# Kernel optimization log

Hardware: AMD Instinct MI355X
Metric: run time of the kernel (lower is better)

The kernel has to match this reference:

```python
import jax, jax.numpy as jnp
import numpy as np

H = 128      # hidden_dim
HEADS = 4
HD = H // HEADS
B, S, D, A, I = 64, 512, 64, 3, 13


def layernorm(x, g, b, eps=1e-5):
    m = x.mean(-1, keepdims=True)
    v = ((x - m) ** 2).mean(-1, keepdims=True)
    return g * (x - m) / jnp.sqrt(v + eps) + b


def setup_inputs() -> dict:
    key = jax.random.key(0)
    ks = jax.random.split(key, 12)
    rn = lambda k, shp, s=0.05: jax.random.normal(k, shp, jnp.float32) * s
    return {
        "x": jax.random.normal(ks[0], (B, S, D), jnp.float32),
        "info": jax.random.normal(ks[1], (B, I), jnp.float32),
        "W_cell": rn(ks[2], (4 * H, D + H)), "b_cell": jnp.zeros(4 * H, jnp.float32),
        "Wqkv": rn(ks[3], (3 * H, H)), "bqkv": jnp.zeros(3 * H, jnp.float32),
        "Wo": rn(ks[4], (H, H)), "bo": jnp.zeros(H, jnp.float32),
        "ln_g": jnp.ones(H, jnp.float32), "ln_b": jnp.zeros(H, jnp.float32),
        "Wa1": rn(ks[5], (128, H + I)), "ba1": jnp.zeros(128, jnp.float32),
        "lna_g": jnp.ones(128, jnp.float32), "lna_b": jnp.zeros(128, jnp.float32),
        "Wa2": rn(ks[6], (A, 128)), "ba2": jnp.zeros(A, jnp.float32),
        "Wc1": rn(ks[7], (128, H + I)), "bc1": jnp.zeros(128, jnp.float32),
        "lnc_g": jnp.ones(128, jnp.float32), "lnc_b": jnp.zeros(128, jnp.float32),
        "Wc2": rn(ks[8], (1, 128)), "bc2": jnp.zeros(1, jnp.float32),
    }


def reference(x, info, W_cell, b_cell, Wqkv, bqkv, Wo, bo, ln_g, ln_b,
              Wa1, ba1, lna_g, lna_b, Wa2, ba2, Wc1, bc1, lnc_g, lnc_b, Wc2, bc2):
    Bx, Sx, _ = x.shape
    h0 = jnp.zeros((Bx, H), x.dtype)
    c0 = jnp.zeros((Bx, H), x.dtype)
    n0 = jnp.ones((Bx, H), x.dtype)

    def step(carry, xt):
        h, c, n = carry
        gates = jnp.concatenate([xt, h], -1) @ W_cell.T + b_cell
        i, f, o, z = jnp.split(gates, 4, axis=-1)
        i = jnp.exp(jnp.clip(i, -5.0, 5.0))
        f = jnp.exp(jnp.clip(f, -5.0, 5.0))
        c = jnp.clip(f * c + i * jnp.tanh(z), -1e6, 1e6)
        n = jnp.clip(f * n + i, 1e-6, 1e6)
        h = jnp.nan_to_num(jax.nn.sigmoid(o) * (c / n), nan=0.0, posinf=0.0, neginf=0.0)
        return (h, c, n), h

    _, hs = jax.lax.scan(step, (h0, c0, n0), jnp.swapaxes(x, 0, 1))  # (S,B,H)
    seq_h = jnp.swapaxes(hs, 0, 1)  # (B,S,H)

    # MultiheadAttention (self-attn, batch_first, shared in_proj)
    qkv = seq_h @ Wqkv.T + bqkv
    q, k, v = jnp.split(qkv, 3, -1)
    split_heads = lambda t: t.reshape(Bx, Sx, HEADS, HD).transpose(0, 2, 1, 3)
    q, k, v = split_heads(q), split_heads(k), split_heads(v)
    scores = jnp.einsum('bhqd,bhkd->bhqk', q, k) / np.sqrt(HD).astype(np.float32)
    attn = jax.nn.softmax(scores, axis=-1)
    av = jnp.einsum('bhqk,bhkd->bhqd', attn, v).transpose(0, 2, 1, 3).reshape(Bx, Sx, H)
    attn_out = av @ Wo.T + bo
    context = layernorm(seq_h + attn_out, ln_g, ln_b).mean(axis=1)  # (B,H)

    comb = jnp.concatenate([context, info], -1)  # (B, H+I)
    action_probs = jax.nn.softmax(
        jax.nn.relu(layernorm(comb @ Wa1.T + ba1, lna_g, lna_b)) @ Wa2.T + ba2, axis=-1)
    value = jax.nn.relu(layernorm(comb @ Wc1.T + bc1, lnc_g, lnc_b)) @ Wc2.T + bc2
    return (action_probs, value)
```

## Files before the change

kernel.cpp:

```cpp
#include <hip/hip_runtime.h>

typedef unsigned short ushort_t;
typedef unsigned int uint_t;

__device__ __forceinline__ float bflo(uint_t u){ union{uint_t i;float f;}v; v.i=u<<16; return v.f; }
__device__ __forceinline__ float bfhi(uint_t u){ union{uint_t i;float f;}v; v.i=u&0xffff0000u; return v.f; }
__device__ __forceinline__ float bfu(ushort_t u){ union{uint_t i;float f;}v; v.i=((uint_t)u)<<16; return v.f; }
__device__ __forceinline__ ushort_t f2b(float f){
  union{float f;uint_t i;}v; v.f=f;
  uint_t r = v.i + 0x7fffu + ((v.i>>16)&1u);
  return (ushort_t)(r>>16);
}
__device__ __forceinline__ void ld8bf(const ushort_t* p, float* w){
  uint4 u = *(const uint4*)p;
  w[0]=bflo(u.x); w[1]=bfhi(u.x); w[2]=bflo(u.y); w[3]=bfhi(u.y);
  w[4]=bflo(u.z); w[5]=bfhi(u.z); w[6]=bflo(u.w); w[7]=bfhi(u.w);
}
__device__ __forceinline__ void cvt8(uint4 u, float* d){
  d[0]=bflo(u.x); d[1]=bfhi(u.x); d[2]=bflo(u.y); d[3]=bfhi(u.y);
  d[4]=bflo(u.z); d[5]=bfhi(u.z); d[6]=bflo(u.w); d[7]=bfhi(u.w);
}
__device__ __forceinline__ float ldin(const void* p, size_t i, int isbf){
  return isbf ? bfu(((const ushort_t*)p)[i]) : ((const float*)p)[i];
}
__device__ __forceinline__ float rlane(float v, int l){
  return __uint_as_float(__builtin_amdgcn_readlane(__float_as_uint(v), l));
}

#define DOT128(acc, Wv, Bv) { float s0_=0.f,s1_=0.f,s2_=0.f,s3_=0.f; \
  _Pragma("unroll") \
  for (int k_=0;k_<128;k_+=4){ float4 h4_ = *(const float4*)&(Bv)[k_]; \
    s0_ += (Wv)[k_]*h4_.x; s1_ += (Wv)[k_+1]*h4_.y; \
    s2_ += (Wv)[k_+2]*h4_.z; s3_ += (Wv)[k_+3]*h4_.w; } \
  acc += (s0_+s1_)+(s2_+s3_); }
#define DOT64A(acc, Wv, Bv) { float s0_=0.f,s1_=0.f,s2_=0.f,s3_=0.f; \
  _Pragma("unroll") \
  for (int k_=0;k_<64;k_+=4){ float4 h4_ = *(const float4*)&(Bv)[k_]; \
    s0_ += (Wv)[k_]*h4_.x; s1_ += (Wv)[k_+1]*h4_.y; \
    s2_ += (Wv)[k_+2]*h4_.z; s3_ += (Wv)[k_+3]*h4_.w; } \
  acc += (s0_+s1_)+(s2_+s3_); }

typedef __attribute__((ext_vector_type(8))) short bf16x8;
typedef __attribute__((ext_vector_type(8))) _Float16 f16x8;
typedef __attribute__((ext_vector_type(4))) float f32x4;
__device__ __forceinline__ bf16x8 bcast8(uint4 u){ return __builtin_bit_cast(bf16x8, u); }
__device__ __forceinline__ f16x8  hcast8(uint4 u){ return __builtin_bit_cast(f16x8, u); }
__device__ __forceinline__ bf16x8 cvt8bf(const float* p){
  float4 a = *(const float4*)p; float4 b = *(const float4*)(p+4);
  uint4 u;
  u.x = (uint_t)f2b(a.x) | ((uint_t)f2b(a.y)<<16);
  u.y = (uint_t)f2b(a.z) | ((uint_t)f2b(a.w)<<16);
  u.z = (uint_t)f2b(b.x) | ((uint_t)f2b(b.y)<<16);
  u.w = (uint_t)f2b(b.z) | ((uint_t)f2b(b.w)<<16);
  return bcast8(u);
}
__device__ __forceinline__ void cvt8hl(const float* p, bf16x8* hi, bf16x8* lo){
  float v[8];
  *(float4*)&v[0] = *(const float4*)p;
  *(float4*)&v[4] = *(const float4*)(p+4);
  ushort_t h[8], l[8];
  #pragma unroll
  for (int j=0;j<8;++j){ h[j] = f2b(v[j]); l[j] = f2b(v[j] - bfu(h[j])); }
  uint4 uh = { (uint_t)h[0]|((uint_t)h[1]<<16), (uint_t)h[2]|((uint_t)h[3]<<16),
               (uint_t)h[4]|((uint_t)h[5]<<16), (uint_t)h[6]|((uint_t)h[7]<<16) };
  uint4 ul = { (uint_t)l[0]|((uint_t)l[1]<<16), (uint_t)l[2]|((uint_t)l[3]<<16),
               (uint_t)l[4]|((uint_t)l[5]<<16), (uint_t)l[6]|((uint_t)l[7]<<16) };
  *hi = bcast8(uh); *lo = bcast8(ul);
}
__device__ __forceinline__ ushort_t f2h(float f){
  _Float16 h = (_Float16)f;
  return __builtin_bit_cast(ushort_t, h);
}
__device__ __forceinline__ float h2f(ushort_t u){
  _Float16 h = __builtin_bit_cast(_Float16, u);
  return (float)h;
}

__global__ void k_detect(const uint_t* __restrict__ lng_raw, int* __restrict__ flag){
  if (threadIdx.x == 0) *flag = (lng_raw[0] == 0x3F803F80u) ? 1 : 0;
}

__global__ __launch_bounds__(256) void k_cvtw(const float* __restrict__ Wq,
    const float* __restrict__ Wo, const float* __restrict__ Wc,
    ushort_t* __restrict__ wqb, ushort_t* __restrict__ wob,
    ushort_t* __restrict__ wxh, ushort_t* __restrict__ wxl,
    ushort_t* __restrict__ whf, ushort_t* __restrict__ whl,
    const int* __restrict__ flag){
  if (*flag == 1) return;
  int i = blockIdx.x*256 + threadIdx.x;
  if (i < 12288){
    float4 f = ((const float4*)Wq)[i];
    uint2 u = { (uint_t)f2b(f.x) | ((uint_t)f2b(f.y)<<16),
                (uint_t)f2b(f.z) | ((uint_t)f2b(f.w)<<16) };
    ((uint2*)wqb)[i] = u;
  } else if (i < 16384){
    int k = i - 12288;
    float4 f = ((const float4*)Wo)[k];
    uint2 u = { (uint_t)f2b(f.x) | ((uint_t)f2b(f.y)<<16),
                (uint_t)f2b(f.z) | ((uint_t)f2b(f.w)<<16) };
    ((uint2*)wob)[k] = u;
  } else if (i < 24576){
    int k = i - 16384;
    int j = k >> 4, kq = (k & 15)*4;
    float4 f = *(const float4*)(Wc + (size_t)j*192 + kq);
    ushort_t h0=f2b(f.x), h1=f2b(f.y), h2=f2b(f.z), h3=f2b(f.w);
    ushort_t l0=f2b(f.x-bfu(h0)), l1=f2b(f.y-bfu(h1));
    ushort_t l2=f2b(f.z-bfu(h2)), l3=f2b(f.w-bfu(h3));
    ((uint2*)(wxh + (size_t)j*64 + kq))[0] = { (uint_t)h0|((uint_t)h1<<16), (uint_t)h2|((uint_t)h3<<16) };
    ((uint2*)(wxl + (size_t)j*64 + kq))[0] = { (uint_t)l0|((uint_t)l1<<16), (uint_t)l2|((uint_t)l3<<16) };
  } else if (i < 32768){
    int k2 = i - 24576;
    int j = k2 >> 4, kc = (k2 & 15)*8;
    const float* src = Wc + (size_t)j*192 + 64 + kc;
    ushort_t hh[8], ll[8];
    #pragma unroll
    for (int q=0;q<8;++q){
      hh[q] = f2h(src[q]);
      ll[q] = f2h(src[q] - h2f(hh[q]));
    }
    uint4 uh = { (uint_t)hh[0]|((uint_t)hh[1]<<16), (uint_t)hh[2]|((uint_t)hh[3]<<16),
                 (uint_t)hh[4]|((uint_t)hh[5]<<16), (uint_t)hh[6]|((uint_t)hh[7]<<16) };
    uint4 ul = { (uint_t)ll[0]|((uint_t)ll[1]<<16), (uint_t)ll[2]|((uint_t)ll[3]<<16),
                 (uint_t)ll[4]|((uint_t)ll[5]<<16), (uint_t)ll[6]|((uint_t)ll[7]<<16) };
    *(uint4*)(whf + (size_t)j*136 + kc) = uh;
    *(uint4*)(whl + (size_t)j*128 + kc) = ul;
  }
}

__global__ __launch_bounds__(256) void k_gx_bf(const void* __restrict__ x,
    const void* __restrict__ Wc, const void* __restrict__ bc,
    float* __restrict__ gx, const int* __restrict__ flag){
  if (*flag == 0) return;
  __shared__ float xs[2048];
  int row0 = blockIdx.x*32, t = threadIdx.x;
  {
    uint4 u = ((const uint4*)((const ushort_t*)x + (size_t)row0*64))[t];
    cvt8(u, &xs[t*8]);
  }
  __syncthreads();
  for (int pass=0; pass<2; ++pass){
    int j = t + pass*256;
    float w[64];
    const ushort_t* wr = (const ushort_t*)Wc + (size_t)j*192;
    #pragma unroll
    for (int q=0;q<8;q++) ld8bf(wr + 8*q, &w[8*q]);
    float bj = bfu(((const ushort_t*)bc)[j]);
    for (int s=0;s<32;++s){
      float acc = bj;
      DOT64A(acc, w, &xs[s*64]);
      gx[(size_t)(row0+s)*512 + j] = acc;
    }
  }
}

__global__ __launch_bounds__(256) void k_gx_f32(const float* __restrict__ x,
    const float* __restrict__ bc,
    const ushort_t* __restrict__ wxh, const ushort_t* __restrict__ wxl,
    float* __restrict__ gx, const int* __restrict__ flag){
  if (*flag == 1) return;
  int t = threadIdx.x, lane = t & 63, wave = t >> 6;
  int l16 = lane & 15, quad = lane >> 4;
  int rowb = blockIdx.x*64 + wave*16;
  const float* xp = x + (size_t)(rowb + l16)*64;
  bf16x8 xh0, xl0, xh1, xl1;
  cvt8hl(xp + quad*8,      &xh0, &xl0);
  cvt8hl(xp + 32 + quad*8, &xh1, &xl1);
  int r0 = rowb + quad*4;
  for (int ct=0; ct<32; ++ct){
    int j = ct*16 + l16;
    const ushort_t* bh = wxh + (size_t)j*64 + quad*8;
    const ushort_t* bl = wxl + (size_t)j*64 + quad*8;
    bf16x8 wh0 = bcast8(*(const uint4*)(bh));
    bf16x8 wh1 = bcast8(*(const uint4*)(bh + 32));
    bf16x8 wl0 = bcast8(*(const uint4*)(bl));
    bf16x8 wl1 = bcast8(*(const uint4*)(bl + 32));
    f32x4 acc = {0.f,0.f,0.f,0.f};
    acc = __builtin_amdgcn_mfma_f32_16x16x32_bf16(xh0, wh0, acc, 0,0,0);
    acc = __builtin_amdgcn_mfma_f32_16x16x32_bf16(xh1, wh1, acc, 0,0,0);
    acc = __builtin_amdgcn_mfma_f32_16x16x32_bf16(xh0, wl0, acc, 0,0,0);
    acc = __builtin_amdgcn_mfma_f32_16x16x32_bf16(xh1, wl1, acc, 0,0,0);
    acc = __builtin_amdgcn_mfma_f32_16x16x32_bf16(xl0, wh0, acc, 0,0,0);
    acc = __builtin_amdgcn_mfma_f32_16x16x32_bf16(xl1, wh1, acc, 0,0,0);
    float bj = bc[j];
    #pragma unroll
    for (int r=0;r<4;++r)
      gx[(size_t)(r0+r)*512 + j] = acc[r] + bj;
  }
}

__global__ __attribute__((amdgpu_flat_work_group_size(512,512), amdgpu_waves_per_eu(2,2)))
void k_rec_hl(const ushort_t* __restrict__ whf,
    const ushort_t* __restrict__ whl,
    const float* __restrict__ gx, float* __restrict__ seq_h,
    const int* __restrict__ flag){
  if (*flag == 1) return;
  int b = blockIdx.x, t = threadIdx.x;
  int lane = t & 63, wv = t >> 6, l16 = lane & 15, quad = lane >> 4;
  __shared__ ushort_t wlds[512*136];
  __shared__ float gs[512];
  __shared__ ushort_t hz[384];
  {
    const uint4* src = (const uint4*)whf;
    uint4* dst = (uint4*)wlds;
    for (int i=t; i<8704; i+=512) dst[i] = src[i];
  }
  if (t < 384) hz[t] = (ushort_t)0;
  const float* gxb = gx + (size_t)b*512*512;
  float g0=0.f,g1=0.f,g2=0.f,g3=0.f;
  float c = 0.f, n = 1.f;
  if (t < 128){
    g0 = gxb[t]; g1 = gxb[128+t]; g2 = gxb[256+t]; g3 = gxb[384+t];
  }
  float* shout = seq_h + (size_t)b*512*128;
  __syncthreads();
  const int c0 = 4*wv, c1 = 4*wv+1, c2 = 4*wv+2, c3 = 4*wv+3;
  const ushort_t* w0 = wlds + (c0*16 + l16)*136 + quad*8;
  const ushort_t* w1 = wlds + (c1*16 + l16)*136 + quad*8;
  const ushort_t* w2 = wlds + (c2*16 + l16)*136 + quad*8;
  const ushort_t* w3 = wlds + (c3*16 + l16)*136 + quad*8;
  const ushort_t* p0 = whl + (size_t)(c0*16 + l16)*128 + quad*8;
  const ushort_t* p1 = whl + (size_t)(c1*16 + l16)*128 + quad*8;
  const ushort_t* p2 = whl + (size_t)(c2*16 + l16)*128 + quad*8;
  const ushort_t* p3 = whl + (size_t)(c3*16 + l16)*128 + quad*8;
#define BDECL(T, ptr) uint4 T##0 = *(const uint4*)(ptr), T##1 = *(const uint4*)((ptr)+32), \
  T##2 = *(const uint4*)((ptr)+64), T##3 = *(const uint4*)((ptr)+96);
  BDECL(U0, w0) BDECL(U1, w1) BDECL(U2, w2) BDECL(U3, w3)
  BDECL(V0, p0) BDECL(V1, p1) BDECL(V2, p2) BDECL(V3, p3)
#undef BDECL
#define UPIN(U) asm volatile("" : "+v"(U.x), "+v"(U.y), "+v"(U.z), "+v"(U.w));
  UPIN(U00) UPIN(U01) UPIN(U02) UPIN(U03)
  UPIN(U10) UPIN(U11) UPIN(U12) UPIN(U13)
  UPIN(U20) UPIN(U21) UPIN(U22) UPIN(U23)
  UPIN(U30) UPIN(U31) UPIN(U32) UPIN(U33)
  UPIN(V00) UPIN(V01) UPIN(V02) UPIN(V03)
  UPIN(V10) UPIN(V11) UPIN(V12) UPIN(V13)
  UPIN(V20) UPIN(V21) UPIN(V22) UPIN(V23)
  UPIN(V30) UPIN(V31) UPIN(V32) UPIN(V33)
#undef UPIN
  const ushort_t* hzsel = hz + ((l16 < 2) ? l16*128 : 256) + quad*8;
  for (int ts=0; ts<512; ++ts){
    f16x8 A0 = hcast8(*(const uint4*)(hzsel));
    f16x8 A1 = hcast8(*(const uint4*)(hzsel + 32));
    f16x8 A2 = hcast8(*(const uint4*)(hzsel + 64));
    f16x8 A3 = hcast8(*(const uint4*)(hzsel + 96));
    f32x4 s0 = {0.f,0.f,0.f,0.f}, s1 = {0.f,0.f,0.f,0.f};
    f32x4 s2 = {0.f,0.f,0.f,0.f}, s3 = {0.f,0.f,0.f,0.f};
#define TILE(sa, Uf, Vf) \
    sa = __builtin_amdgcn_mfma_f32_16x16x32_f16(A0, hcast8(Uf##0), sa, 0,0,0); \
    sa = __builtin_amdgcn_mfma_f32_16x16x32_f16(A1, hcast8(Uf##1), sa, 0,0,0); \
    sa = __builtin_amdgcn_mfma_f32_16x16x32_f16(A2, hcast8(Uf##2), sa, 0,0,0); \
    sa = __builtin_amdgcn_mfma_f32_16x16x32_f16(A3, hcast8(Uf##3), sa, 0,0,0); \
    sa = __builtin_amdgcn_mfma_f32_16x16x32_f16(A0, hcast8(Vf##0), sa, 0,0,0); \
    sa = __builtin_amdgcn_mfma_f32_16x16x32_f16(A1, hcast8(Vf##1), sa, 0,0,0); \
    sa = __builtin_amdgcn_mfma_f32_16x16x32_f16(A2, hcast8(Vf##2), sa, 0,0,0); \
    sa = __builtin_amdgcn_mfma_f32_16x16x32_f16(A3, hcast8(Vf##3), sa, 0,0,0);
    TILE(s0, U0, V0)
    TILE(s1, U1, V1)
    TILE(s2, U2, V2)
    TILE(s3, U3, V3)
#undef TILE
    if (quad == 0){
      gs[c0*16 + l16] = s0[0] + s0[1];
      gs[c1*16 + l16] = s1[0] + s1[1];
      gs[c2*16 + l16] = s2[0] + s2[1];
      gs[c3*16 + l16] = s3[0] + s3[1];
    }
    __syncthreads();
    if (t < 128){
      float gi = gs[t]     + g0;
      float gf = gs[128+t] + g1;
      float go = gs[256+t] + g2;
      float gz = gs[384+t] + g3;
      if (ts+1 < 512){
        const float* gn = gxb + (size_t)(ts+1)*512;
        g0 = gn[t]; g1 = gn[128+t]; g2 = gn[256+t]; g3 = gn[384+t];
      }
      float ii = __expf(fminf(fmaxf(gi,-5.f),5.f));
      float ff = __expf(fminf(fmaxf(gf,-5.f),5.f));
      float e2 = __expf(2.f*gz);
      float zt = 1.f - 2.f/(e2+1.f);
      c = fminf(fmaxf(ff*c + ii*zt, -1e6f), 1e6f);
      n = fminf(fmaxf(ff*n + ii, 1e-6f), 1e6f);
      float oo = 1.f/(1.f+__expf(-go));
      float h = oo*(c/n);
      if (!isfinite(h)) h = 0.f;
      shout[(size_t)ts*128 + t] = h;
      ushort_t hhi = f2h(h);
      hz[t] = hhi;
      hz[128+t] = f2h(h - h2f(hhi));
    }
    __syncthreads();
  }
}

__global__ __launch_bounds__(1024, 4) void k_rec_bf(const void* __restrict__ Wc,
    const float* __restrict__ gx, float* __restrict__ seq_h,
    const int* __restrict__ flag){
  if (*flag == 0) return;
  int b = blockIdx.x, t = threadIdx.x;
  int lane = t & 63, j = t & 511, half = t >> 9;
  __shared__ float ps[1024];
  __shared__ float hs[128];
  uint_t wu[32];
  {
    const uint4* wp = (const uint4*)((const ushort_t*)Wc + (size_t)j*192 + 64 + 64*half);
    #pragma unroll
    for (int q=0;q<8;q++){ uint4 u = wp[q];
      wu[4*q]=u.x; wu[4*q+1]=u.y; wu[4*q+2]=u.z; wu[4*q+3]=u.w; }
  }
  const float* gxb = gx + (size_t)b*512*512;
  float g0=0.f, g1=0.f;
  if (half==0){ g0 = gxb[j]; g1 = gxb[512 + j]; }
  float hreg = 0.f;
  float c = 0.f, n = 1.f;
  float* shout = seq_h + (size_t)b*512*128;
  for (int ts=0; ts<512; ++ts){
    float a0, a1=0.f, a2=0.f, a3=0.f;
    if (half==0){
      a0 = g0; g0 = g1;
      g1 = (ts+2 < 512) ? gxb[(size_t)(ts+2)*512 + j] : 0.f;
    } else a0 = 0.f;
    #pragma unroll
    for (int kk=0; kk<32; kk+=2){
      float h0v = rlane(hreg, 2*kk),   h1v = rlane(hreg, 2*kk+1);
      float h2v = rlane(hreg, 2*kk+2), h3v = rlane(hreg, 2*kk+3);
      a0 = fmaf(bflo(wu[kk]),   h0v, a0);
      a1 = fmaf(bfhi(wu[kk]),   h1v, a1);
      a2 = fmaf(bflo(wu[kk+1]), h2v, a2);
      a3 = fmaf(bfhi(wu[kk+1]), h3v, a3);
    }
    ps[t] = (a0+a1)+(a2+a3);
    __syncthreads();
    if (t < 128){
      float gi = ps[t]     + ps[512+t];
      float gf = ps[128+t] + ps[640+t];
      float go = ps[256+t] + ps[768+t];
      float gz = ps[384+t] + ps[896+t];
      float ii = __expf(fminf(fmaxf(gi,-5.f),5.f));
      float ff = __expf(fminf(fmaxf(gf,-5.f),5.f));
      float e2 = __expf(2.f*gz);
      float zt = 1.f - 2.f/(e2+1.f);
      c = fminf(fmaxf(ff*c + ii*zt, -1e6f), 1e6f);
      n = fminf(fmaxf(ff*n + ii, 1e-6f), 1e6f);
      float oo = 1.f/(1.f+__expf(-go));
      float h = oo*(c/n);
      if (!isfinite(h)) h = 0.f;
      hs[t] = h;
      shout[(size_t)ts*128 + t] = h;
    }
    __syncthreads();
    hreg = hs[(half<<6) | lane];
  }
}

__global__ __launch_bounds__(512) void k_rec_inl(const void* __restrict__ x,
    const void* __restrict__ Wc, const void* __restrict__ bc,
    float* __restrict__ seq_h, const int* __restrict__ flag){
  int isbf = *flag;
  int b = blockIdx.x, j = threadIdx.x;
  __shared__ float hs[128];
  __shared__ float gs[512];
  __shared__ float xr[4][64];
  float w[128], wx[64];
  if (isbf){
    const ushort_t* wr = (const ushort_t*)Wc + (size_t)j*192;
    #pragma unroll
    for (int q=0;q<8;q++)  ld8bf(wr + 8*q, &wx[8*q]);
    #pragma unroll
    for (int q=0;q<16;q++) ld8bf(wr + 64 + 8*q, &w[8*q]);
  } else {
    const float* wr = (const float*)Wc + (size_t)j*192;
    #pragma unroll
    for (int q=0;q<16;q++){ float4 f=*(const float4*)(wr+4*q);
      wx[4*q]=f.x; wx[4*q+1]=f.y; wx[4*q+2]=f.z; wx[4*q+3]=f.w; }
    #pragma unroll
    for (int q=0;q<32;q++){ float4 f=*(const float4*)(wr+64+4*q);
      w[4*q]=f.x; w[4*q+1]=f.y; w[4*q+2]=f.z; w[4*q+3]=f.w; }
  }
  float bj = ldin(bc, j, isbf);
  float c = 0.f, n = 1.f;
  if (j < 128) hs[j] = 0.f;
  if (j < 128){
    int r = j>>6, k = j&63;
    xr[r][k] = ldin(x, ((size_t)b*512 + r)*64 + k, isbf);
  }
  __syncthreads();
  for (int t=0; t<512; ++t){
    const float* xt = xr[t&3];
    float acc = bj;
    DOT64A(acc, wx, xt);
    DOT128(acc, w, hs);
    gs[j] = acc;
    __syncthreads();
    if (j < 128){
      float gi=gs[j], gf=gs[128+j], go=gs[256+j], gz=gs[384+j];
      float ii = __expf(fminf(fmaxf(gi,-5.f),5.f));
      float ff = __expf(fminf(fmaxf(gf,-5.f),5.f));
      float e2 = __expf(2.f*gz);
      float zt = 1.f - 2.f/(e2+1.f);
      c = fminf(fmaxf(ff*c + ii*zt, -1e6f), 1e6f);
      n = fminf(fmaxf(ff*n + ii, 1e-6f), 1e6f);
      float oo = 1.f/(1.f+__expf(-go));
      float h = oo*(c/n);
      if (!isfinite(h)) h = 0.f;
      hs[j] = h;
      seq_h[((size_t)b*512 + t)*128 + j] = h;
    } else if (j >= 448 && (t+2) < 512){
      int k = j & 63;
      xr[(t+2)&3][k] = ldin(x, ((size_t)b*512 + (t+2))*64 + k, isbf);
    }
    __syncthreads();
  }
}

__global__ __launch_bounds__(256) void k_qkv(const float* __restrict__ seq_h,
    const void* __restrict__ Wq, const void* __restrict__ bq,
    const ushort_t* __restrict__ wqb,
    ushort_t* __restrict__ qkv, const int* __restrict__ flag){
  int isbf = *flag;
  int row0 = blockIdx.x*32, t = threadIdx.x;
  if (isbf){
    __shared__ float hsb[4096];
    {
      const float4* hp = (const float4*)(seq_h + (size_t)row0*128);
      #pragma unroll
      for (int i=t;i<1024;i+=256) ((float4*)hsb)[i] = hp[i];
    }
    __syncthreads();
    for (int pass=0; pass<2; ++pass){
      int j = (pass==0) ? t : 256 + t;
      if (j >= 384) break;
      float w[128];
      const ushort_t* wr = (const ushort_t*)Wq + (size_t)j*128;
      #pragma unroll
      for (int q=0;q<16;q++) ld8bf(wr + 8*q, &w[8*q]);
      float bj = bfu(((const ushort_t*)bq)[j]);
      for (int s=0;s<32;++s){
        float acc = bj;
        DOT128(acc, w, &hsb[s*128]);
        qkv[(size_t)(row0+s)*384 + j] = f2b(acc);
      }
    }
  } else {
    int lane = t & 63, wave = t >> 6, l16 = lane & 15, quad = lane >> 4;
    int rt = wave & 1, chalf = wave >> 1;
    int rowg = row0 + rt*16 + l16;
    const float* hp = seq_h + (size_t)rowg*128 + quad*8;
    bf16x8 A0 = cvt8bf(hp);
    bf16x8 A1 = cvt8bf(hp + 32);
    bf16x8 A2 = cvt8bf(hp + 64);
    bf16x8 A3 = cvt8bf(hp + 96);
    int rbase = row0 + rt*16 + quad*4;
    for (int ci=0; ci<12; ++ci){
      int ct = chalf*12 + ci;
      int col = ct*16 + l16;
      const ushort_t* wb = wqb + (size_t)col*128 + quad*8;
      f32x4 acc = {0.f,0.f,0.f,0.f};
      acc = __builtin_amdgcn_mfma_f32_16x16x32_bf16(A0, bcast8(*(const uint4*)(wb)),      acc, 0,0,0);
      acc = __builtin_amdgcn_mfma_f32_16x16x32_bf16(A1, bcast8(*(const uint4*)(wb + 32)), acc, 0,0,0);
      acc = __builtin_amdgcn_mfma_f32_16x16x32_bf16(A2, bcast8(*(const uint4*)(wb + 64)), acc, 0,0,0);
      acc = __builtin_amdgcn_mfma_f32_16x16x32_bf16(A3, bcast8(*(const uint4*)(wb + 96)), acc, 0,0,0);
      float bj = ((const float*)bq)[col];
      #pragma unroll
      for (int r=0;r<4;++r)
        qkv[(size_t)(rbase+r)*384 + col] = f2b(acc[r] + bj);
    }
  }
}

#define AROW4(OP) OP(0) OP(1) OP(2) OP(3)
__global__ __launch_bounds__(512) void k_attn(const ushort_t* __restrict__ qkv,
    ushort_t* __restrict__ av){
  int b = blockIdx.x >> 2, h = blockIdx.x & 3;
  int t = threadIdx.x, lane = t & 63, wave = t >> 6;
  int l16 = lane & 15, quad = lane >> 4;
  __shared__ ushort_t Vt[32*512];
  __shared__ ushort_t Pl[8*16*64];
  const ushort_t* base = qkv + (size_t)b*512*384 + h*32;
  {
    const ushort_t* vr = base + (size_t)t*384 + 256;
    ushort_t tmp[32];
    *(uint4*)&tmp[0]  = *(const uint4*)(vr);
    *(uint4*)&tmp[8]  = *(const uint4*)(vr+8);
    *(uint4*)&tmp[16] = *(const uint4*)(vr+16);
    *(uint4*)&tmp[24] = *(const uint4*)(vr+24);
    #pragma unroll
    for (int d=0; d<32; ++d) Vt[d*512 + t] = tmp[d];
  }
  __syncthreads();
  ushort_t* Pw = Pl + wave*16*64;
  const float scale = 0.17677669529663687f;
  for (int q4=0; q4<4; ++q4){
    int qt = wave + q4*8;
    bf16x8 qa;
    { uint4 u = *(const uint4*)(base + (size_t)(qt*16 + l16)*384 + quad*8);
      qa = bcast8(u); }
    f32x4 O0 = {0.f,0.f,0.f,0.f}, O1 = {0.f,0.f,0.f,0.f};
    float m0=-1e30f,m1=-1e30f,m2=-1e30f,m3=-1e30f;
    float l0=0.f,l1=0.f,l2=0.f,l3=0.f;
    for (int ch=0; ch<8; ++ch){
      f32x4 S0,S1,S2,S3;
      {
        const ushort_t* kb = base + 128 + quad*8;
        uint4 u0 = *(const uint4*)(kb + (size_t)(ch*64 +  0 + l16)*384);
        uint4 u1 = *(const uint4*)(kb + (size_t)(ch*64 + 16 + l16)*384);
        uint4 u2 = *(const uint4*)(kb + (size_t)(ch*64 + 32 + l16)*384);
        uint4 u3 = *(const uint4*)(kb + (size_t)(ch*64 + 48 + l16)*384);
        f32x4 z = {0.f,0.f,0.f,0.f};
        S0 = __builtin_amdgcn_mfma_f32_16x16x32_bf16(qa, bcast8(u0), z, 0,0,0);
        S1 = __builtin_amdgcn_mfma_f32_16x16x32_bf16(qa, bcast8(u1), z, 0,0,0);
        S2 = __builtin_amdgcn_mfma_f32_16x16x32_bf16(qa, bcast8(u2), z, 0,0,0);
        S3 = __builtin_amdgcn_mfma_f32_16x16x32_bf16(qa, bcast8(u3), z, 0,0,0);
      }
#define CMAX(r) float c##r = fmaxf(fmaxf(S0[r],S1[r]), fmaxf(S2[r],S3[r])) * scale; \
      c##r = fmaxf(c##r, __shfl_xor(c##r,1)); c##r = fmaxf(c##r, __shfl_xor(c##r,2)); \
      c##r = fmaxf(c##r, __shfl_xor(c##r,4)); c##r = fmaxf(c##r, __shfl_xor(c##r,8)); \
      float M##r = fmaxf(m##r, c##r); float al##r = __expf(m##r - M##r); \
      m##r = M##r; O0[r] *= al##r; O1[r] *= al##r; l##r *= al##r;
      AROW4(CMAX)
#undef CMAX
#define PEXP(r) float ps##r; { \
      float p0 = __expf(S0[r]*scale - m##r); \
      float p1 = __expf(S1[r]*scale - m##r); \
      float p2 = __expf(S2[r]*scale - m##r); \
      float p3 = __expf(S3[r]*scale - m##r); \
      ps##r = (p0+p1)+(p2+p3); \
      Pw[(quad*4+(r))*64 +  0 + l16] = f2b(p0); \
      Pw[(quad*4+(r))*64 + 16 + l16] = f2b(p1); \
      Pw[(quad*4+(r))*64 + 32 + l16] = f2b(p2); \
      Pw[(quad*4+(r))*64 + 48 + l16] = f2b(p3); }
      AROW4(PEXP)
#undef PEXP
#define PSUM(r) ps##r += __shfl_xor(ps##r,1); ps##r += __shfl_xor(ps##r,2); \
      ps##r += __shfl_xor(ps##r,4); ps##r += __shfl_xor(ps##r,8); l##r += ps##r;
      AROW4(PSUM)
#undef PSUM
      asm volatile("s_waitcnt lgkmcnt(0)" ::: "memory");
      bf16x8 pa0, pa1;
      { uint4 u = *(const uint4*)&Pw[l16*64 + quad*8];      pa0 = bcast8(u); }
      { uint4 u = *(const uint4*)&Pw[l16*64 + 32 + quad*8]; pa1 = bcast8(u); }
      {
        uint4 v0 = *(const uint4*)&Vt[(l16)*512    + ch*64 + quad*8];
        uint4 v1 = *(const uint4*)&Vt[(l16)*512    + ch*64 + 32 + quad*8];
        uint4 v2 = *(const uint4*)&Vt[(16+l16)*512 + ch*64 + quad*8];
        uint4 v3 = *(const uint4*)&Vt[(16+l16)*512 + ch*64 + 32 + quad*8];
        O0 = __builtin_amdgcn_mfma_f32_16x16x32_bf16(pa0, bcast8(v0), O0, 0,0,0);
        O0 = __builtin_amdgcn_mfma_f32_16x16x32_bf16(pa1, bcast8(v1), O0, 0,0,0);
        O1 = __builtin_amdgcn_mfma_f32_16x16x32_bf16(pa0, bcast8(v2), O1, 0,0,0);
        O1 = __builtin_amdgcn_mfma_f32_16x16x32_bf16(pa1, bcast8(v3), O1, 0,0,0);
      }
    }
#define OST(r) { float iv = 1.f/l##r; int row = qt*16 + quad*4 + (r); \
      ushort_t* op = av + (size_t)(b*512 + row)*128 + h*32; \
      op[l16]      = f2b(O0[r]*iv); \
      op[16 + l16] = f2b(O1[r]*iv); }
    AROW4(OST)
#undef OST
  }
}

__global__ __launch_bounds__(256) void k_ctx(const ushort_t* __restrict__ av,
    const float* __restrict__ seq_h, const void* __restrict__ Wo,
    const void* __restrict__ bo_, const void* __restrict__ lng,
    const void* __restrict__ lnb, const ushort_t* __restrict__ wob,
    float* __restrict__ partial, const int* __restrict__ flag){
  int isbf = *flag;
  __shared__ float rs[4096];
  __shared__ float mrow[32], srow[32];
  __shared__ float halfsum[128];
  int row0 = blockIdx.x*32, t = threadIdx.x;
  int j = t & 127, sh = t >> 7;
  if (isbf){
    __shared__ float avs[4096];
    {
      const uint4* ap = (const uint4*)(av + (size_t)row0*128);
      for (int i=t;i<512;i+=256) cvt8(ap[i], &avs[i*8]);
    }
    __syncthreads();
    float w[128];
    const ushort_t* wr = (const ushort_t*)Wo + (size_t)j*128;
    #pragma unroll
    for (int q=0;q<16;q++) ld8bf(wr + 8*q, &w[8*q]);
    float bj = bfu(((const ushort_t*)bo_)[j]);
    for (int si=0; si<16; ++si){
      int s = sh*16 + si;
      float acc = bj;
      DOT128(acc, w, &avs[s*128]);
      rs[s*128+j] = acc + seq_h[(size_t)(row0+s)*128 + j];
    }
  } else {
    int lane = t & 63, wave = t >> 6, l16 = lane & 15, quad = lane >> 4;
    int rt = wave & 1, chalf = wave >> 1;
    int rowg = row0 + rt*16 + l16;
    const ushort_t* ap = av + (size_t)rowg*128 + quad*8;
    bf16x8 A0 = bcast8(*(const uint4*)(ap));
    bf16x8 A1 = bcast8(*(const uint4*)(ap + 32));
    bf16x8 A2 = bcast8(*(const uint4*)(ap + 64));
    bf16x8 A3 = bcast8(*(const uint4*)(ap + 96));
    int rl0 = rt*16 + quad*4;
    for (int ci=0; ci<4; ++ci){
      int ct = chalf*4 + ci;
      int col = ct*16 + l16;
      const ushort_t* wb = wob + (size_t)col*128 + quad*8;
      f32x4 acc = {0.f,0.f,0.f,0.f};
      acc = __builtin_amdgcn_mfma_f32_16x16x32_bf16(A0, bcast8(*(const uint4*)(wb)),      acc, 0,0,0);
      acc = __builtin_amdgcn_mfma_f32_16x16x32_bf16(A1, bcast8(*(const uint4*)(wb + 32)), acc, 0,0,0);
      acc = __builtin_amdgcn_mfma_f32_16x16x32_bf16(A2, bcast8(*(const uint4*)(wb + 64)), acc, 0,0,0);
      acc = __builtin_amdgcn_mfma_f32_16x16x32_bf16(A3, bcast8(*(const uint4*)(wb + 96)), acc, 0,0,0);
      float bj2 = ((const float*)bo_)[col];
      #pragma unroll
      for (int r=0;r<4;++r){
        int rl = rl0 + r;
        rs[rl*128 + col] = acc[r] + bj2 + seq_h[(size_t)(row0+rl)*128 + col];
      }
    }
  }
  __syncthreads();
  {
    int rr = t>>3, part = t&7;
    float vals[16], sm = 0.f;
    #pragma unroll
    for (int k2=0;k2<16;k2++){ vals[k2] = rs[rr*128 + part + 8*k2]; sm += vals[k2]; }
    sm += __shfl_xor(sm,1); sm += __shfl_xor(sm,2); sm += __shfl_xor(sm,4);
    float mean = sm*(1.f/128.f);
    float vv = 0.f;
    #pragma unroll
    for (int k2=0;k2<16;k2++){ float d = vals[k2]-mean; vv += d*d; }
    vv += __shfl_xor(vv,1); vv += __shfl_xor(vv,2); vv += __shfl_xor(vv,4);
    if (part==0){ mrow[rr]=mean; srow[rr]=rsqrtf(vv*(1.f/128.f)+1e-5f); }
  }
  __syncthreads();
  float g = ldin(lng, j, isbf), bb = ldin(lnb, j, isbf);
  float accs = 0.f;
  for (int si=0; si<16; ++si){
    int s = sh*16 + si;
    accs += g*(rs[s*128+j]-mrow[s])*srow[s] + bb;
  }
  if (sh==0) halfsum[j] = accs;
  __syncthreads();
  if (sh==1){
    int bidx = row0>>9, tile = (row0>>5)&15;
    partial[((size_t)bidx*16 + tile)*128 + j] = halfsum[j] + accs;
  }
}

__global__ __launch_bounds__(128) void k_head(const float* __restrict__ partial,
    const void* __restrict__ info,
    const void* Wa1, const void* ba1, const void* lnag, const void* lnab,
    const void* Wa2, const void* ba2,
    const void* Wc1, const void* bc1, const void* lncg, const void* lncb,
    const void* Wc2, const void* bc2, void* __restrict__ out,
    const int* __restrict__ flag){
  int isbf = *flag;
  int b = blockIdx.x, t = threadIdx.x;
  __shared__ float comb[144];
  __shared__ float red[128];
  __shared__ float uu[128];
  float s = 0.f;
  #pragma unroll
  for (int i=0;i<16;i++) s += partial[((size_t)b*16+i)*128 + t];
  comb[t] = s*(1.f/512.f);
  if (t < 13) comb[128+t] = ldin(info, (size_t)b*13+t, isbf);
  __syncthreads();
  for (int br=0; br<2; ++br){
    const void* W1 = br ? Wc1 : Wa1;
    const void* b1 = br ? bc1 : ba1;
    const void* lg_ = br ? lncg : lnag;
    const void* lb_ = br ? lncb : lnab;
    float a = ldin(b1, t, isbf);
    for (int k=0;k<141;k++) a += ldin(W1, (size_t)t*141+k, isbf)*comb[k];
    red[t] = a; __syncthreads();
    for (int st=64; st>0; st>>=1){ if (t<st) red[t]+=red[t+st]; __syncthreads(); }
    float mean = red[0]*(1.f/128.f);
    __syncthreads();
    float d = a - mean;
    red[t] = d*d; __syncthreads();
    for (int st=64; st>0; st>>=1){ if (t<st) red[t]+=red[t+st]; __syncthreads(); }
    float rstd = rsqrtf(red[0]*(1.f/128.f)+1e-5f);
    __syncthreads();
    float u = ldin(lg_, t, isbf)*d*rstd + ldin(lb_, t, isbf);
    uu[t] = fmaxf(u, 0.f);
    __syncthreads();
    if (br==0){
      if (t < 3){
        float lg2 = ldin(ba2, t, isbf);
        for (int k=0;k<128;k++) lg2 += ldin(Wa2, (size_t)t*128+k, isbf)*uu[k];
        red[t] = lg2;
      }
      __syncthreads();
      if (t==0){
        float mx = fmaxf(red[0], fmaxf(red[1], red[2]));
        float e0=__expf(red[0]-mx), e1=__expf(red[1]-mx), e2=__expf(red[2]-mx);
        float inv = 1.f/(e0+e1+e2);
        if (isbf){
          ushort_t* o = (ushort_t*)out;
          o[b*3+0]=f2b(e0*inv); o[b*3+1]=f2b(e1*inv); o[b*3+2]=f2b(e2*inv);
        } else {
          float* o = (float*)out;
          o[b*3+0]=e0*inv; o[b*3+1]=e1*inv; o[b*3+2]=e2*inv;
        }
      }
      __syncthreads();
    } else {
      if (t==0){
        float v = ldin(bc2, 0, isbf);
        for (int k=0;k<128;k++) v += ldin(Wc2, k, isbf)*uu[k];
        if (isbf) ((ushort_t*)out)[192 + b] = f2b(v);
        else      ((float*)out)[192 + b] = v;
      }
    }
  }
}

extern "C" void kernel_launch(void* const* d_in, const int* in_sizes, int n_in,
                              void* d_out, int out_size, void* d_ws, size_t ws_size,
                              hipStream_t stream){
  const void* x    = d_in[0];
  const void* info = d_in[1];
  const void* Wcell= d_in[2];
  const void* bcell= d_in[3];
  const void* Wqkv = d_in[4];
  const void* bqkv = d_in[5];
  const void* Wo   = d_in[6];
  const void* bo   = d_in[7];
  const void* lng  = d_in[8];
  const void* lnb  = d_in[9];
  const void* Wa1  = d_in[10];
  const void* ba1  = d_in[11];
  const void* lnag = d_in[12];
  const void* lnab = d_in[13];
  const void* Wa2  = d_in[14];
  const void* ba2  = d_in[15];
  const void* Wc1  = d_in[16];
  const void* bc1  = d_in[17];
  const void* lncg = d_in[18];
  const void* lncb = d_in[19];
  const void* Wc2  = d_in[20];
  const void* bc2  = d_in[21];

  char* ws = (char*)d_ws;
  const int bigws = (ws_size >= ((size_t)82<<20)) ? 1 : 0;
  float*    seqh = (float*)   ws;
  float*    gxf  = (float*)   (ws + ((size_t)16<<20));
  ushort_t* qkv  = (ushort_t*)(ws + ((size_t)16<<20));
  ushort_t* av   = (ushort_t*)(ws + ((size_t)40<<20));
  float*    part = (float*)   (ws + ((size_t)48<<20));
  int*      flag = bigws ? (int*)(ws + ((size_t)80<<20))
                         : (int*)(ws + ((size_t)48<<20) + (512<<10));
  ushort_t* wqb  = (ushort_t*)(ws + ((size_t)80<<20) + (1<<20));
  ushort_t* wob  = wqb + 384*128;
  ushort_t* wxh  = wob + 128*128;
  ushort_t* wxl  = wxh + 512*64;
  ushort_t* whf  = wxl + 512*64;
  ushort_t* whl  = whf + 512*136;

  k_detect<<<1, 64, 0, stream>>>((const uint_t*)lng, flag);
  if (bigws){
    k_cvtw  <<< 128, 256, 0, stream>>>((const float*)Wqkv, (const float*)Wo,
                                       (const float*)Wcell, wqb, wob, wxh, wxl, whf, whl, flag);
    k_gx_bf <<<1024, 256, 0, stream>>>(x, Wcell, bcell, gxf, flag);
    k_gx_f32<<< 512, 256, 0, stream>>>((const float*)x, (const float*)bcell,
                                       wxh, wxl, gxf, flag);
    k_rec_bf <<< 64, 1024, 0, stream>>>(Wcell, gxf, seqh, flag);
    k_rec_hl <<< 64,  512, 0, stream>>>(whf, whl, gxf, seqh, flag);
  } else {
    k_rec_inl<<<64, 512, 0, stream>>>(x, Wcell, bcell, seqh, flag);
    k_cvtw  <<< 128, 256, 0, stream>>>((const float*)Wqkv, (const float*)Wo,
                                       (const float*)Wcell, wqb, wob, wxh, wxl, whf, whl, flag);
  }
  k_qkv <<<1024, 256, 0, stream>>>(seqh, Wqkv, bqkv, wqb, qkv, flag);
  k_attn<<< 256, 512, 0, stream>>>(qkv, av);
  k_ctx <<<1024, 256, 0, stream>>>(av, seqh, Wo, bo, lng, lnb, wob, part, flag);
  k_head<<<  64, 128, 0, stream>>>(part, info, Wa1, ba1, lnag, lnab, Wa2, ba2,
                                   Wc1, bc1, lncg, lncb, Wc2, bc2, d_out, flag);
}
```

Measured before the change: 736.1 us.

## Replicate recurrent cell update per wave to drop second barrier per step

```diff
diff --git a/kernel.cpp b/kernel.cpp
--- a/kernel.cpp
+++ b/kernel.cpp
@@ -197,31 +197,33 @@
   int b = blockIdx.x, t = threadIdx.x;
   int lane = t & 63, wv = t >> 6, l16 = lane & 15, quad = lane >> 4;
   __shared__ ushort_t wlds[512*136];
-  __shared__ float gs[512];
-  __shared__ ushort_t hz[384];
+  __shared__ float gs[2][512];
+  __shared__ ushort_t hzw[8][448];
   {
     const uint4* src = (const uint4*)whf;
     uint4* dst = (uint4*)wlds;
     for (int i=t; i<8704; i+=512) dst[i] = src[i];
   }
-  if (t < 384) hz[t] = (ushort_t)0;
+  {
+    ushort_t* mz = hzw[wv];
+    for (int i=lane; i<448; i+=64) mz[i] = (ushort_t)0;
+  }
   const float* gxb = gx + (size_t)b*512*512;
-  float g0=0.f,g1=0.f,g2=0.f,g3=0.f;
-  float c = 0.f, n = 1.f;
-  if (t < 128){
-    g0 = gxb[t]; g1 = gxb[128+t]; g2 = gxb[256+t]; g3 = gxb[384+t];
-  }
+  const int i0 = lane, i1 = 64 + lane;
+  float g00=gxb[i0], g01=gxb[128+i0], g02=gxb[256+i0], g03=gxb[384+i0];
+  float g10=gxb[i1], g11=gxb[128+i1], g12=gxb[256+i1], g13=gxb[384+i1];
+  float c0s=0.f, n0s=1.f, c1s=0.f, n1s=1.f;
   float* shout = seq_h + (size_t)b*512*128;
   __syncthreads();
-  const int c0 = 4*wv, c1 = 4*wv+1, c2 = 4*wv+2, c3 = 4*wv+3;
-  const ushort_t* w0 = wlds + (c0*16 + l16)*136 + quad*8;
-  const ushort_t* w1 = wlds + (c1*16 + l16)*136 + quad*8;
-  const ushort_t* w2 = wlds + (c2*16 + l16)*136 + quad*8;
-  const ushort_t* w3 = wlds + (c3*16 + l16)*136 + quad*8;
-  const ushort_t* p0 = whl + (size_t)(c0*16 + l16)*128 + quad*8;
-  const ushort_t* p1 = whl + (size_t)(c1*16 + l16)*128 + quad*8;
-  const ushort_t* p2 = whl + (size_t)(c2*16 + l16)*128 + quad*8;
-  const ushort_t* p3 = whl + (size_t)(c3*16 + l16)*128 + quad*8;
+  const int cc0 = 4*wv, cc1 = 4*wv+1, cc2 = 4*wv+2, cc3 = 4*wv+3;
+  const ushort_t* w0 = wlds + (cc0*16 + l16)*136 + quad*8;
+  const ushort_t* w1 = wlds + (cc1*16 + l16)*136 + quad*8;
+  const ushort_t* w2 = wlds + (cc2*16 + l16)*136 + quad*8;
+  const ushort_t* w3 = wlds + (cc3*16 + l16)*136 + quad*8;
+  const ushort_t* p0 = whl + (size_t)(cc0*16 + l16)*128 + quad*8;
+  const ushort_t* p1 = whl + (size_t)(cc1*16 + l16)*128 + quad*8;
+  const ushort_t* p2 = whl + (size_t)(cc2*16 + l16)*128 + quad*8;
+  const ushort_t* p3 = whl + (size_t)(cc3*16 + l16)*128 + quad*8;
 #define BDECL(T, ptr) uint4 T##0 = *(const uint4*)(ptr), T##1 = *(const uint4*)((ptr)+32), \
   T##2 = *(const uint4*)((ptr)+64), T##3 = *(const uint4*)((ptr)+96);
   BDECL(U0, w0) BDECL(U1, w1) BDECL(U2, w2) BDECL(U3, w3)
@@ -237,7 +239,8 @@
   UPIN(V20) UPIN(V21) UPIN(V22) UPIN(V23)
   UPIN(V30) UPIN(V31) UPIN(V32) UPIN(V33)
 #undef UPIN
-  const ushort_t* hzsel = hz + ((l16 < 2) ? l16*128 : 256) + quad*8;
+  ushort_t* myhz = hzw[wv];
+  const ushort_t* hzsel = myhz + ((l16 == 0) ? 0 : ((l16 == 1) ? 160 : 320)) + quad*8;
   for (int ts=0; ts<512; ++ts){
     f16x8 A0 = hcast8(*(const uint4*)(hzsel));
     f16x8 A1 = hcast8(*(const uint4*)(hzsel + 32));
@@ -260,36 +263,59 @@
     TILE(s3, U3, V3)
 #undef TILE
     if (quad == 0){
-      gs[c0*16 + l16] = s0[0] + s0[1];
-      gs[c1*16 + l16] = s1[0] + s1[1];
-      gs[c2*16 + l16] = s2[0] + s2[1];
-      gs[c3*16 + l16] = s3[0] + s3[1];
-    }
-    __syncthreads();
-    if (t < 128){
-      float gi = gs[t]     + g0;
-      float gf = gs[128+t] + g1;
-      float go = gs[256+t] + g2;
-      float gz = gs[384+t] + g3;
-      if (ts+1 < 512){
-        const float* gn = gxb + (size_t)(ts+1)*512;
-        g0 = gn[t]; g1 = gn[128+t]; g2 = gn[256+t]; g3 = gn[384+t];
-      }
-      float ii = __expf(fminf(fmaxf(gi,-5.f),5.f));
-      float ff = __expf(fminf(fmaxf(gf,-5.f),5.f));
-      float e2 = __expf(2.f*gz);
+      float* go = gs[ts&1];
+      go[cc0*16 + l16] = s0[0] + s0[1];
+      go[cc1*16 + l16] = s1[0] + s1[1];
+      go[cc2*16 + l16] = s2[0] + s2[1];
+      go[cc3*16 + l16] = s3[0] + s3[1];
+    }
+    __syncthreads();
+    const float* gsr = gs[ts&1];
+    float gi0 = gsr[i0]     + g00;
+    float gf0 = gsr[128+i0] + g01;
+    float go0 = gsr[256+i0] + g02;
+    float gz0 = gsr[384+i0] + g03;
+    float gi1 = gsr[i1]     + g10;
+    float gf1 = gsr[128+i1] + g11;
+    float go1 = gsr[256+i1] + g12;
+    float gz1 = gsr[384+i1] + g13;
+    if (ts+1 < 512){
+      const float* gn = gxb + (size_t)(ts+1)*512;
+      g00 = gn[i0]; g01 = gn[128+i0]; g02 = gn[256+i0]; g03 = gn[384+i0];
+      g10 = gn[i1]; g11 = gn[128+i1]; g12 = gn[256+i1]; g13 = gn[384+i1];
+    }
+    float h0, h1;
+    {
+      float ii = __expf(fminf(fmaxf(gi0,-5.f),5.f));
+      float ff = __expf(fminf(fmaxf(gf0,-5.f),5.f));
+      float e2 = __expf(2.f*gz0);
       float zt = 1.f - 2.f/(e2+1.f);
-      c = fminf(fmaxf(ff*c + ii*zt, -1e6f), 1e6f);
-      n = fminf(fmaxf(ff*n + ii, 1e-6f), 1e6f);
-      float oo = 1.f/(1.f+__expf(-go));
-      float h = oo*(c/n);
-      if (!isfinite(h)) h = 0.f;
-      shout[(size_t)ts*128 + t] = h;
-      ushort_t hhi = f2h(h);
-      hz[t] = hhi;
-      hz[128+t] = f2h(h - h2f(hhi));
-    }
-    __syncthreads();
+      c0s = fminf(fmaxf(ff*c0s + ii*zt, -1e6f), 1e6f);
+      n0s = fminf(fmaxf(ff*n0s + ii, 1e-6f), 1e6f);
+      float oo = 1.f/(1.f+__expf(-go0));
+      h0 = oo*(c0s/n0s);
+      if (!isfinite(h0)) h0 = 0.f;
+    }
+    {
+      float ii = __expf(fminf(fmaxf(gi1,-5.f),5.f));
+      float ff = __expf(fminf(fmaxf(gf1,-5.f),5.f));
+      float e2 = __expf(2.f*gz1);
+      float zt = 1.f - 2.f/(e2+1.f);
+      c1s = fminf(fmaxf(ff*c1s + ii*zt, -1e6f), 1e6f);
+      n1s = fminf(fmaxf(ff*n1s + ii, 1e-6f), 1e6f);
+      float oo = 1.f/(1.f+__expf(-go1));
+      h1 = oo*(c1s/n1s);
+      if (!isfinite(h1)) h1 = 0.f;
+    }
+    if (wv == 0){
+      shout[(size_t)ts*128 + i0] = h0;
+      shout[(size_t)ts*128 + i1] = h1;
+    }
+    ushort_t h0h = f2h(h0), h1h = f2h(h1);
+    myhz[i0]       = h0h;
+    myhz[i1]       = h1h;
+    myhz[160 + i0] = f2h(h0 - h2f(h0h));
+    myhz[160 + i1] = f2h(h1 - h2f(h1h));
   }
 }
 
```

Result: slower. 883.0 us (+20.0%).
